# Optimization experiments

Measured on AMD Instinct MI355X. Metric: run time of the kernel, lower is better.

## Reference

```python
import jax, jax.numpy as jnp
import numpy as np

B, T, C, HS = 4, 4096, 1024, 64


def setup_inputs() -> dict:
    key = jax.random.key(0)
    kx, kq, kk, kv = jax.random.split(key, 4)
    x = jax.random.normal(kx, (B, T, C), dtype=jnp.float32)
    s = 1.0 / np.sqrt(C)
    Wq = jax.random.normal(kq, (C, HS), dtype=jnp.float32) * s
    Wk = jax.random.normal(kk, (C, HS), dtype=jnp.float32) * s
    Wv = jax.random.normal(kv, (C, HS), dtype=jnp.float32) * s
    return {"x": x, "Wq": Wq, "Wk": Wk, "Wv": Wv}


def reference(x, Wq, Wk, Wv):
    # q,k,v: [B, T, HS]
    q = x @ Wq
    k = x @ Wk
    v = x @ Wv
    scale = k.shape[-1] ** -0.5
    # full T x T causal attention scores, as the torch module materializes
    scores = jnp.einsum('bqh,bkh->bqk', q, k) * scale  # [B, T, T]
    t = x.shape[1]
    causal = jnp.tril(jnp.ones((t, t), dtype=bool))
    scores = jnp.where(causal[None, :, :], scores, -jnp.inf)
    wei = jax.nn.softmax(scores, axis=-1)  # dropout = 0.0 (eval)
    out = jnp.einsum('bqk,bkh->bqh', wei, v)  # [B, T, HS]
    return out
```

## Files before the change

kernel.cpp:

```cpp
#include <hip/hip_runtime.h>
#include <math.h>

#define BB 4
#define TT 4096
#define CC 1024
#define HS 64
#define MM (BB*TT)

typedef __attribute__((ext_vector_type(8))) short short8;
typedef __attribute__((ext_vector_type(4))) short short4v;
typedef __attribute__((ext_vector_type(4))) float f32x4;
typedef __attribute__((ext_vector_type(4))) unsigned short ushort4v;

__device__ __forceinline__ unsigned short f2bf(float f) {
    union { float f; unsigned u; } v; v.f = f;
    return (unsigned short)((v.u + 0x7fffu + ((v.u >> 16) & 1u)) >> 16);
}

__global__ __launch_bounds__(256) void prep_kernel(
    const float* __restrict__ Wq, const float* __restrict__ Wk,
    const float* __restrict__ Wv, unsigned short* __restrict__ Wfrag)
{
    const int nt = blockIdx.x;
    const int which = nt >> 2;
    const int n0 = (nt & 3) * 16;
    const float* __restrict__ W = (which == 0) ? Wq : (which == 1) ? Wk : Wv;
    const float scale = (which == 0) ? 0.125f : 1.0f;
    const int t = threadIdx.x;
    #pragma unroll
    for (int i = 0; i < 64; i++) {
        int flat = t + 256 * i;
        int k = flat >> 4, c = flat & 15;
        float v = W[(size_t)k * 64 + n0 + c] * scale;
        int ks = k >> 5, quad = (k >> 3) & 3, j = k & 7;
        Wfrag[(((size_t)nt * 32 + ks) * 64 + quad * 16 + c) * 8 + j] = f2bf(v);
    }
}

__global__ __launch_bounds__(256, 2) void qkv_mfma(
    const float* __restrict__ x, const unsigned short* __restrict__ Wfrag,
    unsigned short* __restrict__ qb, unsigned short* __restrict__ kb,
    unsigned short* __restrict__ vT)
{
    const int rt = blockIdx.x;
    __shared__ unsigned short xs[2][32][72];

    const int t = threadIdx.x;
    const int w = t >> 6;
    const int lane = t & 63;
    const int quad = lane >> 4;
    const int c = lane & 15;

    const unsigned short* wfb[3];
    #pragma unroll
    for (int jj = 0; jj < 3; jj++)
        wfb[jj] = Wfrag + ((size_t)(3 * w + jj) * 32 * 64 + lane) * 8;

    float4 xreg[2];
    #pragma unroll
    for (int i = 0; i < 2; i++) {
        int idx = t + 256 * i;
        xreg[i] = *(const float4*)(x + (size_t)(rt * 32 + (idx >> 4)) * CC + (idx & 15) * 4);
    }
    short8 wf[3][2];
    #pragma unroll
    for (int jj = 0; jj < 3; jj++)
        #pragma unroll
        for (int ks2 = 0; ks2 < 2; ks2++)
            wf[jj][ks2] = *(const short8*)(wfb[jj] + ks2 * 512);

    f32x4 acc[2][3];
    #pragma unroll
    for (int mt = 0; mt < 2; mt++)
        #pragma unroll
        for (int jj = 0; jj < 3; jj++) acc[mt][jj] = (f32x4){0.f, 0.f, 0.f, 0.f};

    for (int k0 = 0; k0 < CC; k0 += 64) {
        const int p = (k0 >> 6) & 1;
        #pragma unroll
        for (int i = 0; i < 2; i++) {
            int idx = t + 256 * i;
            int r = idx >> 4, c4 = (idx & 15) * 4;
            ushort4v pk = { f2bf(xreg[i].x), f2bf(xreg[i].y), f2bf(xreg[i].z), f2bf(xreg[i].w) };
            *(ushort4v*)&xs[p][r][c4] = pk;
        }
        if (k0 + 64 < CC) {
            #pragma unroll
            for (int i = 0; i < 2; i++) {
                int idx = t + 256 * i;
                xreg[i] = *(const float4*)(x + (size_t)(rt * 32 + (idx >> 4)) * CC + k0 + 64 + (idx & 15) * 4);
            }
        }
        __syncthreads();
        short8 wn[3][2];
        if (k0 + 64 < CC) {
            #pragma unroll
            for (int jj = 0; jj < 3; jj++)
                #pragma unroll
                for (int ks2 = 0; ks2 < 2; ks2++)
                    wn[jj][ks2] = *(const short8*)(wfb[jj] + ((k0 >> 5) + 2 + ks2) * 512);
        }
        #pragma unroll
        for (int ks2 = 0; ks2 < 2; ks2++) {
            short8 af[2];
            #pragma unroll
            for (int mt = 0; mt < 2; mt++)
                af[mt] = *(const short8*)&xs[p][16 * mt + c][ks2 * 32 + quad * 8];
            #pragma unroll
            for (int mt = 0; mt < 2; mt++)
                #pragma unroll
                for (int jj = 0; jj < 3; jj++)
                    acc[mt][jj] = __builtin_amdgcn_mfma_f32_16x16x32_bf16(af[mt], wf[jj][ks2], acc[mt][jj], 0, 0, 0);
        }
        if (k0 + 64 < CC) {
            #pragma unroll
            for (int jj = 0; jj < 3; jj++)
                #pragma unroll
                for (int ks2 = 0; ks2 < 2; ks2++)
                    wf[jj][ks2] = wn[jj][ks2];
        }
    }

    __syncthreads();
    unsigned short (*vtb)[36] = (unsigned short (*)[36])xs;
    #pragma unroll
    for (int jj = 0; jj < 3; jj++) {
        const int n = 3 * w + jj;
        const int which = n >> 2;
        const int col0 = (n & 3) * 16;
        #pragma unroll
        for (int mt = 0; mt < 2; mt++) {
            #pragma unroll
            for (int reg = 0; reg < 4; reg++) {
                int lrow = 16 * mt + quad * 4 + reg;
                if (which == 0)
                    qb[(size_t)(rt * 32 + lrow) * HS + col0 + c] = f2bf(acc[mt][jj][reg]);
                else if (which == 1)
                    kb[(size_t)(rt * 32 + lrow) * HS + col0 + c] = f2bf(acc[mt][jj][reg]);
                else
                    vtb[col0 + c][lrow] = f2bf(acc[mt][jj][reg]);
            }
        }
    }
    __syncthreads();
    {
        const int b  = rt >> 7;
        const int t0 = (rt & 127) * 32;
        int d = t >> 2, c8 = (t & 3) * 8;
        *(short8*)(vT + ((size_t)b * HS + d) * TT + t0 + c8) = *(const short8*)&vtb[d][c8];
    }
}

__global__ __launch_bounds__(256, 4) void attn_mfma(
    const unsigned short* __restrict__ qb, const unsigned short* __restrict__ kb,
    const unsigned short* __restrict__ vT, float* __restrict__ Opart,
    float* __restrict__ lpart)
{
    const int bid = blockIdx.x;
    const int qt = (TT / 64 - 1) - (bid >> 4);
    const int j  = (bid >> 2) & 3;
    const int b  = bid & 3;

    __shared__ unsigned short ks[64][72];
    __shared__ unsigned short vt[64][72];

    const int t = threadIdx.x;
    const int w = t >> 6;
    const int lane = t & 63;
    const int quad = lane >> 4;
    const int c = lane & 15;
    const int qrow = qt * 64 + 16 * w;

    short8 aq[2];
    #pragma unroll
    for (int ksd = 0; ksd < 2; ksd++)
        aq[ksd] = *(const short8*)(qb + (size_t)(b * TT + qrow + c) * HS + ksd * 32 + quad * 8);

    const int nkt = (qt >= j) ? ((qt - j) >> 2) + 1 : 0;
    const unsigned short* Kb = kb + (size_t)b * TT * HS;
    const unsigned short* Vb = vT + (size_t)b * HS * TT;

    short8 kreg[2], vreg[2];
    if (nkt > 0) {
        const int kt0 = j * 64;
        #pragma unroll
        for (int i = 0; i < 2; i++) {
            int idx = t + 256 * i;
            int row = idx >> 3, c8 = (idx & 7) * 8;
            kreg[i] = *(const short8*)(Kb + (size_t)(kt0 + row) * HS + c8);
            vreg[i] = *(const short8*)(Vb + (size_t)row * TT + kt0 + c8);
        }
    }

    float lsum = 0.f;
    f32x4 oacc[4];
    #pragma unroll
    for (int dt = 0; dt < 4; dt++) oacc[dt] = (f32x4){0.f, 0.f, 0.f, 0.f};

    for (int it = 0; it < nkt; it++) {
        const int kt0 = (j + 4 * it) * 64;
        __syncthreads();
        #pragma unroll
        for (int i = 0; i < 2; i++) {
            int idx = t + 256 * i;
            int row = idx >> 3, c8 = (idx & 7) * 8;
            *(short8*)&ks[row][c8] = kreg[i];
            int t32 = c8 & 32, r32 = c8 & 31;
            int p0 = t32 + ((r32 & 8) << 1) + ((r32 >> 4) << 2);
            short8 v = vreg[i];
            short4v lo = { v[0], v[1], v[2], v[3] };
            short4v hi = { v[4], v[5], v[6], v[7] };
            *(short4v*)&vt[row][p0]     = lo;
            *(short4v*)&vt[row][p0 + 8] = hi;
        }
        if (it + 1 < nkt) {
            const int nb = kt0 + 256;
            #pragma unroll
            for (int i = 0; i < 2; i++) {
                int idx = t + 256 * i;
                int row = idx >> 3, c8 = (idx & 7) * 8;
                kreg[i] = *(const short8*)(Kb + (size_t)(nb + row) * HS + c8);
                vreg[i] = *(const short8*)(Vb + (size_t)row * TT + nb + c8);
            }
        }
        __syncthreads();

        if (kt0 <= qrow + 15) {
            f32x4 sc[4];
            #pragma unroll
            for (int st = 0; st < 4; st++) sc[st] = (f32x4){0.f, 0.f, 0.f, 0.f};
            #pragma unroll
            for (int ksd = 0; ksd < 2; ksd++) {
                short8 kf[4];
                #pragma unroll
                for (int st = 0; st < 4; st++)
                    kf[st] = *(const short8*)&ks[16 * st + c][ksd * 32 + quad * 8];
                #pragma unroll
                for (int st = 0; st < 4; st++)
                    sc[st] = __builtin_amdgcn_mfma_f32_16x16x32_bf16(kf[st], aq[ksd], sc[st], 0, 0, 0);
            }
            const bool needmask = (kt0 + 63 > qrow);
            #pragma unroll
            for (int st = 0; st < 4; st++)
                #pragma unroll
                for (int reg = 0; reg < 4; reg++) {
                    float p;
                    if (needmask) {
                        int key = kt0 + 16 * st + quad * 4 + reg;
                        int qg  = qrow + c;
                        p = (key <= qg) ? __expf(sc[st][reg]) : 0.f;
                    } else {
                        p = __expf(sc[st][reg]);
                    }
                    sc[st][reg] = p;
                    lsum += p;
                }
            short8 pf[2];
            #pragma unroll
            for (int t32 = 0; t32 < 2; t32++) {
                short8 pk;
                #pragma unroll
                for (int reg = 0; reg < 4; reg++) {
                    pk[reg]     = (short)f2bf(sc[2 * t32][reg]);
                    pk[reg + 4] = (short)f2bf(sc[2 * t32 + 1][reg]);
                }
                pf[t32] = pk;
            }
            #pragma unroll
            for (int t32 = 0; t32 < 2; t32++) {
                short8 vf[4];
                #pragma unroll
                for (int dt = 0; dt < 4; dt++)
                    vf[dt] = *(const short8*)&vt[16 * dt + c][t32 * 32 + quad * 8];
                #pragma unroll
                for (int dt = 0; dt < 4; dt++)
                    oacc[dt] = __builtin_amdgcn_mfma_f32_16x16x32_bf16(vf[dt], pf[t32], oacc[dt], 0, 0, 0);
            }
        }
    }

    lsum += __shfl_xor(lsum, 16);
    lsum += __shfl_xor(lsum, 32);

    float* __restrict__ Oj = Opart + (size_t)(j * 4 + b) * HS * TT;
    #pragma unroll
    for (int dt = 0; dt < 4; dt++)
        #pragma unroll
        for (int reg = 0; reg < 4; reg++) {
            int d = 16 * dt + quad * 4 + reg;
            Oj[(size_t)d * TT + qrow + c] = oacc[dt][reg];
        }
    if (lane < 16)
        lpart[(size_t)(j * 4 + b) * TT + qrow + lane] = lsum;
}

__global__ __launch_bounds__(256) void combine_kernel(
    const float* __restrict__ Opart, const float* __restrict__ lpart,
    float* __restrict__ out)
{
    const int b  = blockIdx.x & 3;
    const int q0 = (blockIdx.x >> 2) * 32;
    __shared__ float ts[64][37];
    const int t = threadIdx.x;

    float4 s[2] = {};
    #pragma unroll
    for (int jj = 0; jj < 4; jj++) {
        const float* Oj = Opart + (size_t)(jj * 4 + b) * HS * TT;
        #pragma unroll
        for (int i = 0; i < 2; i++) {
            int idx = t + 256 * i;
            int d = idx >> 3, c4 = (idx & 7) * 4;
            float4 v = *(const float4*)(Oj + (size_t)d * TT + q0 + c4);
            s[i].x += v.x; s[i].y += v.y; s[i].z += v.z; s[i].w += v.w;
        }
    }
    #pragma unroll
    for (int i = 0; i < 2; i++) {
        int idx = t + 256 * i;
        int d = idx >> 3, c4 = (idx & 7) * 4;
        ts[d][c4 + 0] = s[i].x; ts[d][c4 + 1] = s[i].y;
        ts[d][c4 + 2] = s[i].z; ts[d][c4 + 3] = s[i].w;
    }
    __syncthreads();

    const int q  = t >> 3;
    const int dc = (t & 7) * 8;
    float l = 0.f;
    #pragma unroll
    for (int jj = 0; jj < 4; jj++)
        l += lpart[(size_t)(jj * 4 + b) * TT + q0 + q];
    const float inv = 1.f / l;
    float4 r0, r1;
    r0.x = ts[dc + 0][q] * inv; r0.y = ts[dc + 1][q] * inv;
    r0.z = ts[dc + 2][q] * inv; r0.w = ts[dc + 3][q] * inv;
    r1.x = ts[dc + 4][q] * inv; r1.y = ts[dc + 5][q] * inv;
    r1.z = ts[dc + 6][q] * inv; r1.w = ts[dc + 7][q] * inv;
    float* ob = out + (size_t)(b * TT + q0 + q) * HS + dc;
    *(float4*)ob = r0;
    *(float4*)(ob + 4) = r1;
}

extern "C" void kernel_launch(void* const* d_in, const int* in_sizes, int n_in,
                              void* d_out, int out_size, void* d_ws, size_t ws_size,
                              hipStream_t stream) {
    const float* x  = (const float*)d_in[0];
    const float* Wq = (const float*)d_in[1];
    const float* Wk = (const float*)d_in[2];
    const float* Wv = (const float*)d_in[3];
    float* out = (float*)d_out;

    unsigned short* Wfrag = (unsigned short*)d_ws;
    unsigned short* qbuf = Wfrag + 3 * 64 * 1024;
    unsigned short* kbuf = qbuf + (size_t)MM * HS;
    unsigned short* vTb  = kbuf + (size_t)MM * HS;
    float* Opart = (float*)(vTb + (size_t)MM * HS);
    float* lpart = Opart + 4 * (size_t)MM * HS;

    prep_kernel<<<12, 256, 0, stream>>>(Wq, Wk, Wv, Wfrag);
    qkv_mfma<<<MM / 32, 256, 0, stream>>>(x, Wfrag, qbuf, kbuf, vTb);
    attn_mfma<<<BB * (TT / 64) * 4, 256, 0, stream>>>(qbuf, kbuf, vTb, Opart, lpart);
    combine_kernel<<<BB * (TT / 32), 256, 0, stream>>>(Opart, lpart, out);
}
```

Baseline: 143.7 us.

## Double K-step tiles in QKV and attention, use exp2 and packed bf16 conversion

The QKV projection now stages 128 input columns per iteration instead of 64, which halves the number of barriers and loop trips. The attention kernel stages two 64-key tiles per barrier pair, using a 128-row K buffer and a wider V buffer. The log2(e) factor is folded into the Q weight scale so the softmax can call exp2f, and pairs of floats are converted to bf16 with the packed intrinsic. In exchange the kernels use more LDS and registers, which may lower occupancy, and when the tile count is odd the clamped prefetch loads a redundant tile.

```diff
diff --git a/kernel.cpp b/kernel.cpp
--- a/kernel.cpp
+++ b/kernel.cpp
@@ -1,4 +1,5 @@
 #include <hip/hip_runtime.h>
+#include <hip/hip_bf16.h>
 #include <math.h>
 
 #define BB 4
@@ -10,11 +11,14 @@
 typedef __attribute__((ext_vector_type(8))) short short8;
 typedef __attribute__((ext_vector_type(4))) short short4v;
 typedef __attribute__((ext_vector_type(4))) float f32x4;
-typedef __attribute__((ext_vector_type(4))) unsigned short ushort4v;
 
 __device__ __forceinline__ unsigned short f2bf(float f) {
     union { float f; unsigned u; } v; v.f = f;
     return (unsigned short)((v.u + 0x7fffu + ((v.u >> 16) & 1u)) >> 16);
+}
+__device__ __forceinline__ unsigned pk2bf(float a, float b) {
+    __hip_bfloat162 h = __float22bfloat162_rn(float2{a, b});
+    union { __hip_bfloat162 h2; unsigned u; } v; v.h2 = h; return v.u;
 }
 
 __global__ __launch_bounds__(256) void prep_kernel(
@@ -25,7 +29,7 @@
     const int which = nt >> 2;
     const int n0 = (nt & 3) * 16;
     const float* __restrict__ W = (which == 0) ? Wq : (which == 1) ? Wk : Wv;
-    const float scale = (which == 0) ? 0.125f : 1.0f;
+    const float scale = (which == 0) ? 0.18033688f : 1.0f;
     const int t = threadIdx.x;
     #pragma unroll
     for (int i = 0; i < 64; i++) {
@@ -43,7 +47,7 @@
     unsigned short* __restrict__ vT)
 {
     const int rt = blockIdx.x;
-    __shared__ unsigned short xs[2][32][72];
+    __shared__ unsigned short xs[2][32][136];
 
     const int t = threadIdx.x;
     const int w = t >> 6;
@@ -56,17 +60,17 @@
     for (int jj = 0; jj < 3; jj++)
         wfb[jj] = Wfrag + ((size_t)(3 * w + jj) * 32 * 64 + lane) * 8;
 
-    float4 xreg[2];
-    #pragma unroll
-    for (int i = 0; i < 2; i++) {
+    float4 xreg[4];
+    #pragma unroll
+    for (int i = 0; i < 4; i++) {
         int idx = t + 256 * i;
-        xreg[i] = *(const float4*)(x + (size_t)(rt * 32 + (idx >> 4)) * CC + (idx & 15) * 4);
-    }
-    short8 wf[3][2];
+        xreg[i] = *(const float4*)(x + (size_t)(rt * 32 + (idx >> 5)) * CC + (idx & 31) * 4);
+    }
+    short8 wf[3][4];
     #pragma unroll
     for (int jj = 0; jj < 3; jj++)
         #pragma unroll
-        for (int ks2 = 0; ks2 < 2; ks2++)
+        for (int ks2 = 0; ks2 < 4; ks2++)
             wf[jj][ks2] = *(const short8*)(wfb[jj] + ks2 * 512);
 
     f32x4 acc[2][3];
@@ -75,33 +79,34 @@
         #pragma unroll
         for (int jj = 0; jj < 3; jj++) acc[mt][jj] = (f32x4){0.f, 0.f, 0.f, 0.f};
 
-    for (int k0 = 0; k0 < CC; k0 += 64) {
-        const int p = (k0 >> 6) & 1;
-        #pragma unroll
-        for (int i = 0; i < 2; i++) {
+    for (int k0 = 0; k0 < CC; k0 += 128) {
+        const int p = (k0 >> 7) & 1;
+        #pragma unroll
+        for (int i = 0; i < 4; i++) {
             int idx = t + 256 * i;
-            int r = idx >> 4, c4 = (idx & 15) * 4;
-            ushort4v pk = { f2bf(xreg[i].x), f2bf(xreg[i].y), f2bf(xreg[i].z), f2bf(xreg[i].w) };
-            *(ushort4v*)&xs[p][r][c4] = pk;
-        }
-        if (k0 + 64 < CC) {
-            #pragma unroll
-            for (int i = 0; i < 2; i++) {
+            int r = idx >> 5, c4 = (idx & 31) * 4;
+            unsigned lo = pk2bf(xreg[i].x, xreg[i].y);
+            unsigned hi = pk2bf(xreg[i].z, xreg[i].w);
+            *(uint2*)&xs[p][r][c4] = make_uint2(lo, hi);
+        }
+        if (k0 + 128 < CC) {
+            #pragma unroll
+            for (int i = 0; i < 4; i++) {
                 int idx = t + 256 * i;
-                xreg[i] = *(const float4*)(x + (size_t)(rt * 32 + (idx >> 4)) * CC + k0 + 64 + (idx & 15) * 4);
+                xreg[i] = *(const float4*)(x + (size_t)(rt * 32 + (idx >> 5)) * CC + k0 + 128 + (idx & 31) * 4);
             }
         }
         __syncthreads();
-        short8 wn[3][2];
-        if (k0 + 64 < CC) {
+        short8 wn[3][4];
+        if (k0 + 128 < CC) {
             #pragma unroll
             for (int jj = 0; jj < 3; jj++)
                 #pragma unroll
-                for (int ks2 = 0; ks2 < 2; ks2++)
-                    wn[jj][ks2] = *(const short8*)(wfb[jj] + ((k0 >> 5) + 2 + ks2) * 512);
-        }
-        #pragma unroll
-        for (int ks2 = 0; ks2 < 2; ks2++) {
+                for (int ks2 = 0; ks2 < 4; ks2++)
+                    wn[jj][ks2] = *(const short8*)(wfb[jj] + ((k0 >> 5) + 4 + ks2) * 512);
+        }
+        #pragma unroll
+        for (int ks2 = 0; ks2 < 4; ks2++) {
             short8 af[2];
             #pragma unroll
             for (int mt = 0; mt < 2; mt++)
@@ -112,11 +117,11 @@
                 for (int jj = 0; jj < 3; jj++)
                     acc[mt][jj] = __builtin_amdgcn_mfma_f32_16x16x32_bf16(af[mt], wf[jj][ks2], acc[mt][jj], 0, 0, 0);
         }
-        if (k0 + 64 < CC) {
+        if (k0 + 128 < CC) {
             #pragma unroll
             for (int jj = 0; jj < 3; jj++)
                 #pragma unroll
-                for (int ks2 = 0; ks2 < 2; ks2++)
+                for (int ks2 = 0; ks2 < 4; ks2++)
                     wf[jj][ks2] = wn[jj][ks2];
         }
     }
@@ -161,8 +166,8 @@
     const int j  = (bid >> 2) & 3;
     const int b  = bid & 3;
 
-    __shared__ unsigned short ks[64][72];
-    __shared__ unsigned short vt[64][72];
+    __shared__ unsigned short ks[128][72];
+    __shared__ unsigned short vt[64][136];
 
     const int t = threadIdx.x;
     const int w = t >> 6;
@@ -177,104 +182,110 @@
         aq[ksd] = *(const short8*)(qb + (size_t)(b * TT + qrow + c) * HS + ksd * 32 + quad * 8);
 
     const int nkt = (qt >= j) ? ((qt - j) >> 2) + 1 : 0;
+    const int nsi = (nkt + 1) >> 1;
     const unsigned short* Kb = kb + (size_t)b * TT * HS;
     const unsigned short* Vb = vT + (size_t)b * HS * TT;
 
-    short8 kreg[2], vreg[2];
-    if (nkt > 0) {
-        const int kt0 = j * 64;
-        #pragma unroll
-        for (int i = 0; i < 2; i++) {
-            int idx = t + 256 * i;
-            int row = idx >> 3, c8 = (idx & 7) * 8;
-            kreg[i] = *(const short8*)(Kb + (size_t)(kt0 + row) * HS + c8);
-            vreg[i] = *(const short8*)(Vb + (size_t)row * TT + kt0 + c8);
-        }
-    }
-
-    float lsum = 0.f;
-    f32x4 oacc[4];
-    #pragma unroll
-    for (int dt = 0; dt < 4; dt++) oacc[dt] = (f32x4){0.f, 0.f, 0.f, 0.f};
-
-    for (int it = 0; it < nkt; it++) {
-        const int kt0 = (j + 4 * it) * 64;
-        __syncthreads();
-        #pragma unroll
-        for (int i = 0; i < 2; i++) {
-            int idx = t + 256 * i;
-            int row = idx >> 3, c8 = (idx & 7) * 8;
-            *(short8*)&ks[row][c8] = kreg[i];
-            int t32 = c8 & 32, r32 = c8 & 31;
-            int p0 = t32 + ((r32 & 8) << 1) + ((r32 >> 4) << 2);
-            short8 v = vreg[i];
-            short4v lo = { v[0], v[1], v[2], v[3] };
-            short4v hi = { v[4], v[5], v[6], v[7] };
-            *(short4v*)&vt[row][p0]     = lo;
-            *(short4v*)&vt[row][p0 + 8] = hi;
-        }
-        if (it + 1 < nkt) {
-            const int nb = kt0 + 256;
+    short8 kreg[2][2], vreg[2][2];
+    if (nsi > 0) {
+        #pragma unroll
+        for (int h = 0; h < 2; h++) {
+            const int ti = min(j + 4 * h, TT / 64 - 1);
             #pragma unroll
             for (int i = 0; i < 2; i++) {
                 int idx = t + 256 * i;
                 int row = idx >> 3, c8 = (idx & 7) * 8;
-                kreg[i] = *(const short8*)(Kb + (size_t)(nb + row) * HS + c8);
-                vreg[i] = *(const short8*)(Vb + (size_t)row * TT + nb + c8);
-            }
-        }
+                kreg[h][i] = *(const short8*)(Kb + (size_t)(ti * 64 + row) * HS + c8);
+                vreg[h][i] = *(const short8*)(Vb + (size_t)row * TT + ti * 64 + c8);
+            }
+        }
+    }
+
+    float lsum = 0.f;
+    f32x4 oacc[4];
+    #pragma unroll
+    for (int dt = 0; dt < 4; dt++) oacc[dt] = (f32x4){0.f, 0.f, 0.f, 0.f};
+
+    for (int si = 0; si < nsi; si++) {
         __syncthreads();
-
-        if (kt0 <= qrow + 15) {
-            f32x4 sc[4];
-            #pragma unroll
-            for (int st = 0; st < 4; st++) sc[st] = (f32x4){0.f, 0.f, 0.f, 0.f};
-            #pragma unroll
-            for (int ksd = 0; ksd < 2; ksd++) {
-                short8 kf[4];
+        #pragma unroll
+        for (int h = 0; h < 2; h++)
+            #pragma unroll
+            for (int i = 0; i < 2; i++) {
+                int idx = t + 256 * i;
+                int row = idx >> 3, c8 = (idx & 7) * 8;
+                *(short8*)&ks[64 * h + row][c8] = kreg[h][i];
+                int g32 = 2 * h + (c8 >> 5);
+                int r32 = c8 & 31;
+                int p0 = g32 * 32 + ((r32 & 8) << 1) + ((r32 >> 4) << 2);
+                short8 v = vreg[h][i];
+                short4v lo = { v[0], v[1], v[2], v[3] };
+                short4v hi = { v[4], v[5], v[6], v[7] };
+                *(short4v*)&vt[row][p0]     = lo;
+                *(short4v*)&vt[row][p0 + 8] = hi;
+            }
+        if (si + 1 < nsi) {
+            #pragma unroll
+            for (int h = 0; h < 2; h++) {
+                const int ti = min(j + 8 * (si + 1) + 4 * h, TT / 64 - 1);
+                #pragma unroll
+                for (int i = 0; i < 2; i++) {
+                    int idx = t + 256 * i;
+                    int row = idx >> 3, c8 = (idx & 7) * 8;
+                    kreg[h][i] = *(const short8*)(Kb + (size_t)(ti * 64 + row) * HS + c8);
+                    vreg[h][i] = *(const short8*)(Vb + (size_t)row * TT + ti * 64 + c8);
+                }
+            }
+        }
+        __syncthreads();
+
+        #pragma unroll
+        for (int h = 0; h < 2; h++) {
+            const int kt0 = (j + 8 * si + 4 * h) * 64;
+            if (kt0 <= qrow + 15) {
+                f32x4 sc[4];
+                #pragma unroll
+                for (int st = 0; st < 4; st++) sc[st] = (f32x4){0.f, 0.f, 0.f, 0.f};
+                #pragma unroll
+                for (int ksd = 0; ksd < 2; ksd++) {
+                    short8 kf[4];
+                    #pragma unroll
+                    for (int st = 0; st < 4; st++)
+                        kf[st] = *(const short8*)&ks[64 * h + 16 * st + c][ksd * 32 + quad * 8];
+                    #pragma unroll
+                    for (int st = 0; st < 4; st++)
+                        sc[st] = __builtin_amdgcn_mfma_f32_16x16x32_bf16(kf[st], aq[ksd], sc[st], 0, 0, 0);
+                }
+                const bool needmask = (kt0 + 63 > qrow);
                 #pragma unroll
                 for (int st = 0; st < 4; st++)
-                    kf[st] = *(const short8*)&ks[16 * st + c][ksd * 32 + quad * 8];
-                #pragma unroll
-                for (int st = 0; st < 4; st++)
-                    sc[st] = __builtin_amdgcn_mfma_f32_16x16x32_bf16(kf[st], aq[ksd], sc[st], 0, 0, 0);
-            }
-            const bool needmask = (kt0 + 63 > qrow);
-            #pragma unroll
-            for (int st = 0; st < 4; st++)
-                #pragma unroll
-                for (int reg = 0; reg < 4; reg++) {
-                    float p;
-                    if (needmask) {
-                        int key = kt0 + 16 * st + quad * 4 + reg;
-                        int qg  = qrow + c;
-                        p = (key <= qg) ? __expf(sc[st][reg]) : 0.f;
-                    } else {
-                        p = __expf(sc[st][reg]);
+                    #pragma unroll
+                    for (int reg = 0; reg < 4; reg++) {
+                        float p;
+                        if (needmask) {
+                            int key = kt0 + 16 * st + quad * 4 + reg;
+                            p = (key <= qrow + c) ? exp2f(sc[st][reg]) : 0.f;
+                        } else {
+                            p = exp2f(sc[st][reg]);
+                        }
+                        sc[st][reg] = p;
+                        lsum += p;
                     }
-                    sc[st][reg] = p;
-                    lsum += p;
+                #pragma unroll
+                for (int t32 = 0; t32 < 2; t32++) {
+                    union { short8 s8; unsigned u[4]; } pu;
+                    pu.u[0] = pk2bf(sc[2 * t32 + 0][0], sc[2 * t32 + 0][1]);
+                    pu.u[1] = pk2bf(sc[2 * t32 + 0][2], sc[2 * t32 + 0][3]);
+                    pu.u[2] = pk2bf(sc[2 * t32 + 1][0], sc[2 * t32 + 1][1]);
+                    pu.u[3] = pk2bf(sc[2 * t32 + 1][2], sc[2 * t32 + 1][3]);
+                    short8 vf[4];
+                    #pragma unroll
+                    for (int dt = 0; dt < 4; dt++)
+                        vf[dt] = *(const short8*)&vt[16 * dt + c][(2 * h + t32) * 32 + quad * 8];
+                    #pragma unroll
+                    for (int dt = 0; dt < 4; dt++)
+                        oacc[dt] = __builtin_amdgcn_mfma_f32_16x16x32_bf16(vf[dt], pu.s8, oacc[dt], 0, 0, 0);
                 }
-            short8 pf[2];
-            #pragma unroll
-            for (int t32 = 0; t32 < 2; t32++) {
-                short8 pk;
-                #pragma unroll
-                for (int reg = 0; reg < 4; reg++) {
-                    pk[reg]     = (short)f2bf(sc[2 * t32][reg]);
-                    pk[reg + 4] = (short)f2bf(sc[2 * t32 + 1][reg]);
-                }
-                pf[t32] = pk;
-            }
-            #pragma unroll
-            for (int t32 = 0; t32 < 2; t32++) {
-                short8 vf[4];
-                #pragma unroll
-                for (int dt = 0; dt < 4; dt++)
-                    vf[dt] = *(const short8*)&vt[16 * dt + c][t32 * 32 + quad * 8];
-                #pragma unroll
-                for (int dt = 0; dt < 4; dt++)
-                    oacc[dt] = __builtin_amdgcn_mfma_f32_16x16x32_bf16(vf[dt], pf[t32], oacc[dt], 0, 0, 0);
             }
         }
     }
```

After: 141.4 us. Within noise of the previous version (-1.6%).
